# Optimization experiments

Measured on AMD Instinct MI355X. Metric: run time of the kernel, lower is better.

## Reference

```python
import jax, jax.numpy as jnp
import numpy as np
import math


def setup_inputs() -> dict:
    rng = jax.random.key(0)
    k1, k2, k3 = jax.random.split(rng, 3)
    B, L, H, E = 2, 1024, 8, 64
    query = jax.random.normal(k1, (B, L, H, E), dtype=jnp.float32)
    key = jax.random.normal(k2, (B, L, H, E), dtype=jnp.float32)
    value = jax.random.normal(k3, (B, L, H, E), dtype=jnp.float32)
    mask_miss_k = jnp.zeros((B, L), dtype=bool)
    mask_miss_q = jnp.zeros((B, L), dtype=bool)
    pos = jnp.arange(B * L).reshape(B, L)
    causal_mask = 0  # unused by the module body
    # learned scalar parameters (nn.Parameter init values)
    log_gain_gate = jnp.float32(math.log(2.0))
    log_tau_gate = jnp.float32(math.log(0.5))
    log_gain_dir = jnp.float32(math.log(3.0))
    log_tau_dir = jnp.float32(math.log(0.3))
    return {
        "query": query, "key": key, "value": value,
        "mask_miss_k": mask_miss_k, "mask_miss_q": mask_miss_q,
        "pos": pos, "causal_mask": causal_mask,
        "log_gain_gate": log_gain_gate, "log_tau_gate": log_tau_gate,
        "log_gain_dir": log_gain_dir, "log_tau_dir": log_tau_dir,
    }


def reference(query, key, value, mask_miss_k, mask_miss_q, pos, causal_mask,
              log_gain_gate, log_tau_gate, log_gain_dir, log_tau_dir):
    # Multihead path: query (B,L,H,E). Eval mode, dropout p=0, dag_mask=None.
    B, L, H, E = query.shape
    scale = 1.0 / jnp.sqrt(jnp.float32(E))
    # scores: (B,H,L,S) with S == L
    scores = scale * jnp.einsum('blhe,bshe->bhls', query, key)
    scores_t = jnp.swapaxes(scores, -1, -2)
    S_sym = 0.5 * (scores + scores_t)       # symmetric part
    A_anti = 0.5 * (scores - scores_t)      # antisymmetric (Lie) part

    MAX_GAIN = 20.0
    gain_gate = jnp.clip(jnp.exp(log_gain_gate), 1e-3, MAX_GAIN)
    tau_gate = jnp.clip(jnp.exp(log_tau_gate), 1e-3, 10.0)
    gain_dir = jnp.clip(jnp.exp(log_gain_dir), 1e-3, MAX_GAIN)
    tau_dir = jnp.clip(jnp.exp(log_tau_dir), 1e-3, 10.0)

    gamma_att = gain_gate * jnp.tanh(S_sym / tau_gate)
    phi_att = gain_dir * jnp.tanh(A_anti / tau_dir)

    gate_probs = jax.nn.sigmoid(gamma_att)
    dir_probs = jax.nn.sigmoid(phi_att)
    dag_probs = gate_probs * dir_probs

    diag = jnp.eye(L, L, dtype=bool)  # P(i->i) = 0
    dag_probs = jnp.where(diag[None, None], 0.0, dag_probs)
    M = dag_probs  # eval branch; diagonal already zeroed (second fill is a no-op)

    att = jax.nn.relu(jnp.tanh(A_anti * gain_dir / tau_dir)) * M

    # entropy per query position (B,H,L)
    entropy = -jnp.sum(att * jnp.log(jnp.clip(att, 1e-8, None)), axis=-1)
    entropy = jnp.nan_to_num(entropy)

    # dropout p=0 -> identity; nan_to_num is a no-op on finite att
    V = jnp.einsum('bhls,bshd->blhd', att, value)  # (B,L,H,E)
    return V, att, entropy
```

## Files before the change

### kernel.cpp

```cpp
#include <hip/hip_runtime.h>
#include <math.h>

namespace {

typedef __bf16 bf16_t;
typedef bf16_t bf16x8 __attribute__((ext_vector_type(8)));
typedef bf16_t bf16x4 __attribute__((ext_vector_type(4)));
typedef bf16_t bf16x2 __attribute__((ext_vector_type(2)));
typedef float f32x4 __attribute__((ext_vector_type(4)));

constexpr int L = 1024;
constexpr int H = 8;
constexpr int E = 64;
constexpr int HE = H * E;
constexpr int BH = 16;
constexpr size_t PL = (size_t)BH * L * E;
constexpr float LOG2E = 1.4426950408889634f;
constexpr float LN2 = 0.6931471805599453f;

__device__ __forceinline__ float rcp_fast(float x) { return __builtin_amdgcn_rcpf(x); }
__device__ __forceinline__ float exp2_fast(float x) { return __builtin_amdgcn_exp2f(x); }
__device__ __forceinline__ float log2_fast(float x) { return __builtin_amdgcn_logf(x); }
__device__ __forceinline__ f32x4 mfma16(bf16x8 a, bf16x8 b, f32x4 c) {
  return __builtin_amdgcn_mfma_f32_16x16x32_bf16(a, b, c, 0, 0, 0);
}
__device__ __forceinline__ void split4(float4 x, bf16x4& hv, bf16x4& lv) {
  hv[0] = (bf16_t)x.x; lv[0] = (bf16_t)(x.x - (float)hv[0]);
  hv[1] = (bf16_t)x.y; lv[1] = (bf16_t)(x.y - (float)hv[1]);
  hv[2] = (bf16_t)x.z; lv[2] = (bf16_t)(x.z - (float)hv[2]);
  hv[3] = (bf16_t)x.w; lv[3] = (bf16_t)(x.w - (float)hv[3]);
}

__global__ __launch_bounds__(256) void k_prep(
    const float* __restrict__ q, const float* __restrict__ k,
    const float* __restrict__ v, bf16_t* __restrict__ ws,
    float* __restrict__ Vout, float* __restrict__ entr)
{
  const int bid = blockIdx.x;
  if (bid >= 512) {
    const int idx = (bid - 512) * 256 + threadIdx.x;
    const float4 z = make_float4(0.f, 0.f, 0.f, 0.f);
    if (idx < 262144) *(float4*)(Vout + (size_t)idx * 4) = z;
    else              *(float4*)(entr + (size_t)(idx - 262144) * 4) = z;
    return;
  }
  bf16_t* Qh = ws;
  bf16_t* Ql = ws + PL;
  bf16_t* Kh = ws + 2 * PL;
  bf16_t* Kl = ws + 3 * PL;
  bf16_t* VT = ws + 4 * PL;
  const int bh = bid >> 5, chunk = bid & 31;
  const int b = bh >> 3, h = bh & 7;
  const int tid = threadIdx.x, t8 = tid >> 4, c4 = tid & 15;
  __shared__ bf16_t Vb[64][40];

#pragma unroll
  for (int pass = 0; pass < 2; ++pass) {
    const int row = chunk * 32 + pass * 16 + t8;
    const size_t gin = ((size_t)(b * L + row) * H + h) * E + c4 * 4;
    const size_t gout = ((size_t)bh * L + row) * E + c4 * 4;
    float4 q4 = *(const float4*)(q + gin);
    float4 k4 = *(const float4*)(k + gin);
    float4 v4 = *(const float4*)(v + gin);
    bf16x4 hv, lv;
    split4(q4, hv, lv);
    *(bf16x4*)(Qh + gout) = hv; *(bf16x4*)(Ql + gout) = lv;
    split4(k4, hv, lv);
    *(bf16x4*)(Kh + gout) = hv; *(bf16x4*)(Kl + gout) = lv;
    const int sl = pass * 16 + t8;
    Vb[c4 * 4 + 0][sl] = (bf16_t)v4.x;
    Vb[c4 * 4 + 1][sl] = (bf16_t)v4.y;
    Vb[c4 * 4 + 2][sl] = (bf16_t)v4.z;
    Vb[c4 * 4 + 3][sl] = (bf16_t)v4.w;
  }
  __syncthreads();
  {
    const int e = tid >> 2, ch = tid & 3;
    bf16x8 val = *(const bf16x8*)&Vb[e][ch * 8];
    *(bf16x8*)(VT + ((size_t)bh * E + e) * L + chunk * 32 + ch * 8) = val;
  }
}

__global__ __launch_bounds__(256, 3) void k_main(
    const bf16_t* __restrict__ ws,
    float* __restrict__ Vout, float* __restrict__ attg, float* __restrict__ entr,
    const float* __restrict__ p_lgg, const float* __restrict__ p_ltg,
    const float* __restrict__ p_lgd, const float* __restrict__ p_ltd)
{
  const bf16_t* Qh = ws;
  const bf16_t* Ql = ws + PL;
  const bf16_t* Kh = ws + 2 * PL;
  const bf16_t* Kl = ws + 3 * PL;
  const bf16_t* VT = ws + 4 * PL;

  __shared__ __align__(16) char smem[51200];
  bf16_t (*Kh_s)[72] = (bf16_t(*)[72])(smem);
  bf16_t (*Kl_s)[72] = (bf16_t(*)[72])(smem + 9216);
  bf16_t (*Qh_s)[72] = (bf16_t(*)[72])(smem + 18432);
  bf16_t (*Ql_s)[72] = (bf16_t(*)[72])(smem + 27648);
  bf16_t (*Vt_s)[72] = (bf16_t(*)[72])(smem + 36864);
  bf16_t (*attL)[40] = (bf16_t(*)[40])(smem + 46080);

  const int tid = threadIdx.x;
  const int w = tid >> 6, lane = tid & 63;
  const int c = lane & 15, qd = lane >> 4;
  const int lh = w & 1, sh = w >> 1;
  const int wid = blockIdx.x;
  const int xcd = wid & 7, slot = wid >> 3;
  const int bh = xcd * 2 + (slot >> 7);
  const int rsl = slot & 127;
  const int lt = rsl & 31, zb = rsl >> 5;
  const int b = bh >> 3, h = bh & 7;
  const int l0 = lt * 32;

  const float gg = fminf(fmaxf(__expf(p_lgg[0]), 1e-3f), 20.0f);
  const float tg = fminf(fmaxf(__expf(p_ltg[0]), 1e-3f), 10.0f);
  const float gd = fminf(fmaxf(__expf(p_lgd[0]), 1e-3f), 20.0f);
  const float td = fminf(fmaxf(__expf(p_ltd[0]), 1e-3f), 10.0f);
  const float A1 = 0.125f * (1.0f / tg) * LOG2E;
  const float A2 = 0.125f * (1.0f / td) * LOG2E;
  const float A3 = 0.125f * gd * (1.0f / td) * LOG2E;
  const float G1 = -gg * LOG2E, G1m2 = -2.0f * G1;
  const float G2 = -gd * LOG2E, G2m2 = -2.0f * G2;

  bf16x8 qaf[2][2], kaf[2][2];
  {
    const size_t aro = ((size_t)bh * L + l0 + lh * 16 + c) * E;
#pragma unroll
    for (int ks = 0; ks < 2; ++ks) {
      qaf[ks][0] = *(const bf16x8*)(Qh + aro + ks * 32 + qd * 8);
      qaf[ks][1] = *(const bf16x8*)(Ql + aro + ks * 32 + qd * 8);
      kaf[ks][0] = *(const bf16x8*)(Kh + aro + ks * 32 + qd * 8);
      kaf[ks][1] = *(const bf16x8*)(Kl + aro + ks * 32 + qd * 8);
    }
  }

  const int srow = tid >> 2, scol = (tid & 3) * 16;

  bf16x8 kh8a, kh8b, kl8a, kl8b, qh8a, qh8b, ql8a, ql8b, vt8a, vt8b;
  {
    const int s0 = zb * 4 * 64;
    const size_t off = ((size_t)bh * L + s0 + srow) * E + scol;
    kh8a = *(const bf16x8*)(Kh + off);   kh8b = *(const bf16x8*)(Kh + off + 8);
    kl8a = *(const bf16x8*)(Kl + off);   kl8b = *(const bf16x8*)(Kl + off + 8);
    qh8a = *(const bf16x8*)(Qh + off);   qh8b = *(const bf16x8*)(Qh + off + 8);
    ql8a = *(const bf16x8*)(Ql + off);   ql8b = *(const bf16x8*)(Ql + off + 8);
    const size_t voff = ((size_t)bh * E + srow) * L + s0 + scol;
    vt8a = *(const bf16x8*)(VT + voff);  vt8b = *(const bf16x8*)(VT + voff + 8);
  }

  f32x4 accv[4] = {};
  float ent[4] = {0.f, 0.f, 0.f, 0.f};

#pragma unroll
  for (int it = 0; it < 4; ++it) {
    const int s0 = (zb * 4 + it) * 64;
    const int s0n = ((zb * 4 + it + 1) & 15) * 64;

    __syncthreads();
    *(bf16x8*)&Kh_s[srow][scol]     = kh8a;
    *(bf16x8*)&Kh_s[srow][scol + 8] = kh8b;
    *(bf16x8*)&Kl_s[srow][scol]     = kl8a;
    *(bf16x8*)&Kl_s[srow][scol + 8] = kl8b;
    *(bf16x8*)&Qh_s[srow][scol]     = qh8a;
    *(bf16x8*)&Qh_s[srow][scol + 8] = qh8b;
    *(bf16x8*)&Ql_s[srow][scol]     = ql8a;
    *(bf16x8*)&Ql_s[srow][scol + 8] = ql8b;
    *(bf16x8*)&Vt_s[srow][scol]     = vt8a;
    *(bf16x8*)&Vt_s[srow][scol + 8] = vt8b;
    __syncthreads();

    {
      const size_t off = ((size_t)bh * L + s0n + srow) * E + scol;
      kh8a = *(const bf16x8*)(Kh + off);   kh8b = *(const bf16x8*)(Kh + off + 8);
      kl8a = *(const bf16x8*)(Kl + off);   kl8b = *(const bf16x8*)(Kl + off + 8);
      qh8a = *(const bf16x8*)(Qh + off);   qh8b = *(const bf16x8*)(Qh + off + 8);
      ql8a = *(const bf16x8*)(Ql + off);   ql8b = *(const bf16x8*)(Ql + off + 8);
      const size_t voff = ((size_t)bh * E + srow) * L + s0n + scol;
      vt8a = *(const bf16x8*)(VT + voff);  vt8b = *(const bf16x8*)(VT + voff + 8);
    }

    f32x4 acc1[2] = {}, acc2[2] = {};
#pragma unroll
    for (int nt = 0; nt < 2; ++nt) {
      const int brow = sh * 32 + nt * 16 + c;
#pragma unroll
      for (int ks = 0; ks < 2; ++ks) {
        bf16x8 kbh = *(const bf16x8*)&Kh_s[brow][ks * 32 + qd * 8];
        bf16x8 kbl = *(const bf16x8*)&Kl_s[brow][ks * 32 + qd * 8];
        bf16x8 qbh = *(const bf16x8*)&Qh_s[brow][ks * 32 + qd * 8];
        bf16x8 qbl = *(const bf16x8*)&Ql_s[brow][ks * 32 + qd * 8];
        acc1[nt] = mfma16(qaf[ks][0], kbh, acc1[nt]);
        acc1[nt] = mfma16(qaf[ks][0], kbl, acc1[nt]);
        acc1[nt] = mfma16(qaf[ks][1], kbh, acc1[nt]);
        acc2[nt] = mfma16(kaf[ks][0], qbh, acc2[nt]);
        acc2[nt] = mfma16(kaf[ks][1], qbh, acc2[nt]);
        acc2[nt] = mfma16(kaf[ks][0], qbl, acc2[nt]);
      }
    }

    float* arow = attg + ((size_t)bh * L + l0 + lh * 16 + qd * 4) * L + s0 + sh * 32;
#pragma unroll
    for (int nt = 0; nt < 2; ++nt) {
#pragma unroll
      for (int r = 0; r < 4; ++r) {
        float u = acc1[nt][r] + acc2[nt][r];
        float d = acc1[nt][r] - acc2[nt][r];
        float r1 = rcp_fast(exp2_fast(u * A1) + 1.f);
        float gate = rcp_fast(1.f + exp2_fast(fmaf(r1, G1m2, G1)));
        float r2 = rcp_fast(exp2_fast(d * A2) + 1.f);
        float dir  = rcp_fast(1.f + exp2_fast(fmaf(r2, G2m2, G2)));
        float t    = fmaf(rcp_fast(exp2_fast(d * A3) + 1.f), -2.f, 1.f);
        float a = fmaxf(t, 0.0f) * gate * dir;
        ent[r] -= a * log2_fast(fmaxf(a, 1e-8f));
        __builtin_nontemporal_store(a, arow + (size_t)r * L + nt * 16 + c);
        attL[w * 16 + qd * 4 + r][nt * 16 + c] = (bf16_t)a;
      }
    }
    asm volatile("s_waitcnt lgkmcnt(0)" ::: "memory");

    bf16x8 af = *(const bf16x8*)&attL[w * 16 + c][qd * 8];
#pragma unroll
    for (int ne = 0; ne < 4; ++ne) {
      bf16x8 bv = *(const bf16x8*)&Vt_s[ne * 16 + c][sh * 32 + qd * 8];
      accv[ne] = mfma16(af, bv, accv[ne]);
    }
  }

  __syncthreads();
  float (*red)[68] = (float(*)[68])smem;
  if (sh == 1) {
#pragma unroll
    for (int ne = 0; ne < 4; ++ne)
#pragma unroll
      for (int r = 0; r < 4; ++r)
        red[lh * 16 + qd * 4 + r][ne * 16 + c] = accv[ne][r];
  }
  __syncthreads();
  if (sh == 0) {
#pragma unroll
    for (int ne = 0; ne < 4; ++ne)
#pragma unroll
      for (int r = 0; r < 4; ++r) {
        float val = accv[ne][r] + red[lh * 16 + qd * 4 + r][ne * 16 + c];
        atomicAdd(Vout + ((size_t)(b * L + l0 + lh * 16 + qd * 4 + r) * H + h) * E +
                      ne * 16 + c,
                  val);
      }
  }
#pragma unroll
  for (int r = 0; r < 4; ++r) {
    float e = ent[r];
    e += __shfl_xor(e, 1);
    e += __shfl_xor(e, 2);
    e += __shfl_xor(e, 4);
    e += __shfl_xor(e, 8);
    if (c == 0)
      atomicAdd(entr + (size_t)bh * L + l0 + lh * 16 + qd * 4 + r, e * LN2);
  }
}

__device__ __forceinline__ float tanh_fast(float x) {
  return 1.0f - 2.0f * rcp_fast(__expf(2.0f * x) + 1.0f);
}
__device__ __forceinline__ float sigm_fast(float x) {
  return rcp_fast(1.0f + __expf(-x));
}
__device__ __forceinline__ void split_store(bf16_t* hi, bf16_t* lo, float4 x) {
  bf16x4 hv, lv;
  split4(x, hv, lv);
  *(bf16x4*)hi = hv;
  *(bf16x4*)lo = lv;
}

__global__ __launch_bounds__(128, 1) void fused_attn(
    const float* __restrict__ q, const float* __restrict__ kk,
    const float* __restrict__ v,
    float* __restrict__ Vout, float* __restrict__ attg, float* __restrict__ entr,
    const float* __restrict__ p_lgg, const float* __restrict__ p_ltg,
    const float* __restrict__ p_lgd, const float* __restrict__ p_ltd)
{
  constexpr int TM = 32;
  __shared__ bf16_t Qa_hi[TM][72], Qa_lo[TM][72];
  __shared__ bf16_t Ka_hi[TM][72], Ka_lo[TM][72];
  __shared__ bf16_t KQ_hi[64][72], KQ_lo[64][72];
  __shared__ bf16_t Vts[64][72];
  __shared__ float  T2ex[2][64][17];
  __shared__ bf16_t attLs[2][16][72];

  const int tid = threadIdx.x;
  const int w = tid >> 6;
  const int lane = tid & 63;
  const int c = lane & 15;
  const int qd = lane >> 4;
  const int t8 = tid >> 4;
  const int c4 = tid & 15;
  const int lt = blockIdx.x;
  const int bh = blockIdx.y;
  const int b = bh >> 3, h = bh & 7;
  const int l0 = lt * TM;

  const float gg = fminf(fmaxf(__expf(p_lgg[0]), 1e-3f), 20.0f);
  const float tg = fminf(fmaxf(__expf(p_ltg[0]), 1e-3f), 10.0f);
  const float gd = fminf(fmaxf(__expf(p_lgd[0]), 1e-3f), 20.0f);
  const float td = fminf(fmaxf(__expf(p_ltd[0]), 1e-3f), 10.0f);
  const float inv_tg = 1.0f / tg;
  const float inv_td = 1.0f / td;
  const float gd_inv_td = gd * inv_td;

  const float* qlbase = q  + ((size_t)(b * L + l0) * H + h) * E;
  const float* qsbase = q  + ((size_t)b * L * H + h) * E;
  const float* kbase  = kk + ((size_t)b * L * H + h) * E;
  const float* vbase  = v  + ((size_t)b * L * H + h) * E;

#pragma unroll
  for (int i = 0; i < 4; ++i) {
    int r = t8 + 8 * i;
    float4 qa = *(const float4*)(qlbase + (size_t)r * HE + c4 * 4);
    float4 ka = *(const float4*)(kbase + (size_t)(l0 + r) * HE + c4 * 4);
    split_store(&Qa_hi[r][c4 * 4], &Qa_lo[r][c4 * 4], qa);
    split_store(&Ka_hi[r][c4 * 4], &Ka_lo[r][c4 * 4], ka);
  }

  float4 kpre[8], qpre[8];
  float vpre[32];
#pragma unroll
  for (int i = 0; i < 8; ++i)
    kpre[i] = *(const float4*)(kbase + (size_t)(t8 + 8 * i) * HE + c4 * 4);
#pragma unroll
  for (int i = 0; i < 8; ++i)
    qpre[i] = *(const float4*)(qsbase + (size_t)(t8 + 8 * i) * HE + c4 * 4);
#pragma unroll
  for (int j = 0; j < 32; ++j)
    vpre[j] = vbase[(size_t)(w * 32 + j) * HE + lane];

  __syncthreads();

  bf16x8 qaf[2][2], kaf[2][2];
#pragma unroll
  for (int ks = 0; ks < 2; ++ks) {
    qaf[ks][0] = *(const bf16x8*)&Qa_hi[w * 16 + c][ks * 32 + qd * 8];
    qaf[ks][1] = *(const bf16x8*)&Qa_lo[w * 16 + c][ks * 32 + qd * 8];
    kaf[ks][0] = *(const bf16x8*)&Ka_hi[w * 16 + c][ks * 32 + qd * 8];
    kaf[ks][1] = *(const bf16x8*)&Ka_lo[w * 16 + c][ks * 32 + qd * 8];
  }

  f32x4 accv[4] = {};
  float ent[4] = {0.f, 0.f, 0.f, 0.f};
  const int gl_base = l0 + w * 16 + qd * 4;

  for (int it = 0; it < 16; ++it) {
    const int s0 = it * 64;
    const int snext = ((it + 1) & 15) * 64;

    __syncthreads();
#pragma unroll
    for (int i = 0; i < 8; ++i) {
      int r = t8 + 8 * i;
      split_store(&KQ_hi[r][c4 * 4], &KQ_lo[r][c4 * 4], kpre[i]);
    }
#pragma unroll
    for (int j = 0; j < 16; ++j) {
      bf16x2 p;
      p[0] = (bf16_t)vpre[2 * j];
      p[1] = (bf16_t)vpre[2 * j + 1];
      *(bf16x2*)&Vts[lane][w * 32 + 2 * j] = p;
    }
    __syncthreads();

#pragma unroll
    for (int i = 0; i < 8; ++i)
      kpre[i] = *(const float4*)(kbase + (size_t)(snext + t8 + 8 * i) * HE + c4 * 4);
#pragma unroll
    for (int j = 0; j < 32; ++j)
      vpre[j] = vbase[(size_t)(snext + w * 32 + j) * HE + lane];

    f32x4 acc1[4] = {};
#pragma unroll
    for (int nt = 0; nt < 4; ++nt) {
#pragma unroll
      for (int ks = 0; ks < 2; ++ks) {
        bf16x8 bhv = *(const bf16x8*)&KQ_hi[nt * 16 + c][ks * 32 + qd * 8];
        bf16x8 blv = *(const bf16x8*)&KQ_lo[nt * 16 + c][ks * 32 + qd * 8];
        acc1[nt] = mfma16(qaf[ks][0], bhv, acc1[nt]);
        acc1[nt] = mfma16(qaf[ks][0], blv, acc1[nt]);
        acc1[nt] = mfma16(qaf[ks][1], bhv, acc1[nt]);
      }
    }
    __syncthreads();

#pragma unroll
    for (int i = 0; i < 8; ++i) {
      int r = t8 + 8 * i;
      split_store(&KQ_hi[r][c4 * 4], &KQ_lo[r][c4 * 4], qpre[i]);
    }
    __syncthreads();

#pragma unroll
    for (int i = 0; i < 8; ++i)
      qpre[i] = *(const float4*)(qsbase + (size_t)(snext + t8 + 8 * i) * HE + c4 * 4);

    f32x4 acc2[4] = {};
#pragma unroll
    for (int mt = 0; mt < 4; ++mt) {
#pragma unroll
      for (int ks = 0; ks < 2; ++ks) {
        bf16x8 ahv = *(const bf16x8*)&KQ_hi[mt * 16 + c][ks * 32 + qd * 8];
        bf16x8 alv = *(const bf16x8*)&KQ_lo[mt * 16 + c][ks * 32 + qd * 8];
        acc2[mt] = mfma16(ahv, kaf[ks][0], acc2[mt]);
        acc2[mt] = mfma16(ahv, kaf[ks][1], acc2[mt]);
        acc2[mt] = mfma16(alv, kaf[ks][0], acc2[mt]);
      }
    }

#pragma unroll
    for (int mt = 0; mt < 4; ++mt)
#pragma unroll
      for (int r = 0; r < 4; ++r)
        T2ex[w][mt * 16 + qd * 4 + r][c] = acc2[mt][r];
    __syncthreads();

    float* attrow0 = attg + ((size_t)bh * L + gl_base) * L + s0;
#pragma unroll
    for (int nt = 0; nt < 4; ++nt) {
#pragma unroll
      for (int r = 0; r < 4; ++r) {
        float x = 0.125f * acc1[nt][r];
        float y = 0.125f * T2ex[w][nt * 16 + c][qd * 4 + r];
        float Ss = 0.5f * (x + y);
        float Aa = 0.5f * (x - y);
        float gate = sigm_fast(gg * tanh_fast(Ss * inv_tg));
        float dir  = sigm_fast(gd * tanh_fast(Aa * inv_td));
        float t    = tanh_fast(Aa * gd_inv_td);
        float a = fmaxf(t, 0.0f) * gate * dir;
        ent[r] -= a * __logf(fmaxf(a, 1e-8f));
        attrow0[(size_t)r * L + nt * 16 + c] = a;
        attLs[w][qd * 4 + r][nt * 16 + c] = (bf16_t)a;
      }
    }
    __syncthreads();

#pragma unroll
    for (int ks = 0; ks < 2; ++ks) {
      bf16x8 af = *(const bf16x8*)&attLs[w][c][ks * 32 + qd * 8];
#pragma unroll
      for (int ne = 0; ne < 4; ++ne) {
        bf16x8 bfv = *(const bf16x8*)&Vts[ne * 16 + c][ks * 32 + qd * 8];
        accv[ne] = mfma16(af, bfv, accv[ne]);
      }
    }
  }

#pragma unroll
  for (int r = 0; r < 4; ++r) {
    float* vb = Vout + ((size_t)(b * L + gl_base + r) * H + h) * E;
#pragma unroll
    for (int ne = 0; ne < 4; ++ne) vb[ne * 16 + c] = accv[ne][r];
    float e4 = ent[r];
    e4 += __shfl_xor(e4, 1);
    e4 += __shfl_xor(e4, 2);
    e4 += __shfl_xor(e4, 4);
    e4 += __shfl_xor(e4, 8);
    if (c == 0) entr[(size_t)bh * L + gl_base + r] = e4;
  }
}

}

extern "C" void kernel_launch(void* const* d_in, const int* in_sizes, int n_in,
                              void* d_out, int out_size, void* d_ws, size_t ws_size,
                              hipStream_t stream) {
  const float* q = (const float*)d_in[0];
  const float* k = (const float*)d_in[1];
  const float* v = (const float*)d_in[2];
  const float* p_lgg = (const float*)d_in[7];
  const float* p_ltg = (const float*)d_in[8];
  const float* p_lgd = (const float*)d_in[9];
  const float* p_ltd = (const float*)d_in[10];

  float* Vout = (float*)d_out;
  float* att  = Vout + 1048576;
  float* entr = att + 16777216;

  const size_t need = 5 * PL * sizeof(bf16_t);
  if (ws_size >= need) {
    bf16_t* ws = (bf16_t*)d_ws;
    k_prep<<<dim3(1552), 256, 0, stream>>>(q, k, v, ws, Vout, entr);
    k_main<<<dim3(2048), 256, 0, stream>>>(
        ws, Vout, att, entr, p_lgg, p_ltg, p_lgd, p_ltd);
  } else {
    fused_attn<<<dim3(32, 16), 128, 0, stream>>>(
        q, k, v, Vout, att, entr, p_lgg, p_ltg, p_lgd, p_ltd);
  }
}
```

Before: 140.5 us.

## Drop split-S decomposition in main kernel, write outputs directly without atomics

The main kernel previously split the key dimension across 4 blocks per query tile (2048 blocks) and combined partial V and entropy results with atomicAdd, which required a zeroing pass in the prep kernel. Each block now loops over all 16 key tiles itself, so there are 512 blocks, the V and entropy outputs are written with plain stores, and the zero-fill blocks are removed from k_prep. This removes atomic traffic and the memset work, but each block now runs four times longer and there are fewer blocks to spread across the CUs, so latency hiding and load balance may suffer.

```diff
diff --git a/kernel.cpp b/kernel.cpp
--- a/kernel.cpp
+++ b/kernel.cpp
@@ -33,22 +33,14 @@
 
 __global__ __launch_bounds__(256) void k_prep(
     const float* __restrict__ q, const float* __restrict__ k,
-    const float* __restrict__ v, bf16_t* __restrict__ ws,
-    float* __restrict__ Vout, float* __restrict__ entr)
+    const float* __restrict__ v, bf16_t* __restrict__ ws)
 {
-  const int bid = blockIdx.x;
-  if (bid >= 512) {
-    const int idx = (bid - 512) * 256 + threadIdx.x;
-    const float4 z = make_float4(0.f, 0.f, 0.f, 0.f);
-    if (idx < 262144) *(float4*)(Vout + (size_t)idx * 4) = z;
-    else              *(float4*)(entr + (size_t)(idx - 262144) * 4) = z;
-    return;
-  }
   bf16_t* Qh = ws;
   bf16_t* Ql = ws + PL;
   bf16_t* Kh = ws + 2 * PL;
   bf16_t* Kl = ws + 3 * PL;
   bf16_t* VT = ws + 4 * PL;
+  const int bid = blockIdx.x;
   const int bh = bid >> 5, chunk = bid & 31;
   const int b = bh >> 3, h = bh & 7;
   const int tid = threadIdx.x, t8 = tid >> 4, c4 = tid & 15;
@@ -107,9 +99,8 @@
   const int lh = w & 1, sh = w >> 1;
   const int wid = blockIdx.x;
   const int xcd = wid & 7, slot = wid >> 3;
-  const int bh = xcd * 2 + (slot >> 7);
-  const int rsl = slot & 127;
-  const int lt = rsl & 31, zb = rsl >> 5;
+  const int bh = xcd * 2 + (slot >> 5);
+  const int lt = slot & 31;
   const int b = bh >> 3, h = bh & 7;
   const int l0 = lt * 32;
 
@@ -139,23 +130,21 @@
 
   bf16x8 kh8a, kh8b, kl8a, kl8b, qh8a, qh8b, ql8a, ql8b, vt8a, vt8b;
   {
-    const int s0 = zb * 4 * 64;
-    const size_t off = ((size_t)bh * L + s0 + srow) * E + scol;
+    const size_t off = ((size_t)bh * L + srow) * E + scol;
     kh8a = *(const bf16x8*)(Kh + off);   kh8b = *(const bf16x8*)(Kh + off + 8);
     kl8a = *(const bf16x8*)(Kl + off);   kl8b = *(const bf16x8*)(Kl + off + 8);
     qh8a = *(const bf16x8*)(Qh + off);   qh8b = *(const bf16x8*)(Qh + off + 8);
     ql8a = *(const bf16x8*)(Ql + off);   ql8b = *(const bf16x8*)(Ql + off + 8);
-    const size_t voff = ((size_t)bh * E + srow) * L + s0 + scol;
+    const size_t voff = ((size_t)bh * E + srow) * L + scol;
     vt8a = *(const bf16x8*)(VT + voff);  vt8b = *(const bf16x8*)(VT + voff + 8);
   }
 
   f32x4 accv[4] = {};
   float ent[4] = {0.f, 0.f, 0.f, 0.f};
 
-#pragma unroll
-  for (int it = 0; it < 4; ++it) {
-    const int s0 = (zb * 4 + it) * 64;
-    const int s0n = ((zb * 4 + it + 1) & 15) * 64;
+  for (int it = 0; it < 16; ++it) {
+    const int s0 = it * 64;
+    const int s0n = ((it + 1) & 15) * 64;
 
     __syncthreads();
     *(bf16x8*)&Kh_s[srow][scol]     = kh8a;
@@ -229,25 +218,9 @@
 
   __syncthreads();
   float (*red)[68] = (float(*)[68])smem;
-  if (sh == 1) {
-#pragma unroll
-    for (int ne = 0; ne < 4; ++ne)
-#pragma unroll
-      for (int r = 0; r < 4; ++r)
-        red[lh * 16 + qd * 4 + r][ne * 16 + c] = accv[ne][r];
-  }
-  __syncthreads();
-  if (sh == 0) {
-#pragma unroll
-    for (int ne = 0; ne < 4; ++ne)
-#pragma unroll
-      for (int r = 0; r < 4; ++r) {
-        float val = accv[ne][r] + red[lh * 16 + qd * 4 + r][ne * 16 + c];
-        atomicAdd(Vout + ((size_t)(b * L + l0 + lh * 16 + qd * 4 + r) * H + h) * E +
-                      ne * 16 + c,
-                  val);
-      }
-  }
+  float* entE = (float*)(smem + 12288);
+
+  float er[4];
 #pragma unroll
   for (int r = 0; r < 4; ++r) {
     float e = ent[r];
@@ -255,8 +228,34 @@
     e += __shfl_xor(e, 2);
     e += __shfl_xor(e, 4);
     e += __shfl_xor(e, 8);
+    er[r] = e;
+  }
+  if (sh == 1) {
+#pragma unroll
+    for (int ne = 0; ne < 4; ++ne)
+#pragma unroll
+      for (int r = 0; r < 4; ++r)
+        red[lh * 16 + qd * 4 + r][ne * 16 + c] = accv[ne][r];
     if (c == 0)
-      atomicAdd(entr + (size_t)bh * L + l0 + lh * 16 + qd * 4 + r, e * LN2);
+#pragma unroll
+      for (int r = 0; r < 4; ++r)
+        entE[lh * 16 + qd * 4 + r] = er[r];
+  }
+  __syncthreads();
+  if (sh == 0) {
+#pragma unroll
+    for (int ne = 0; ne < 4; ++ne)
+#pragma unroll
+      for (int r = 0; r < 4; ++r) {
+        float val = accv[ne][r] + red[lh * 16 + qd * 4 + r][ne * 16 + c];
+        Vout[((size_t)(b * L + l0 + lh * 16 + qd * 4 + r) * H + h) * E +
+             ne * 16 + c] = val;
+      }
+    if (c == 0)
+#pragma unroll
+      for (int r = 0; r < 4; ++r)
+        entr[(size_t)bh * L + l0 + lh * 16 + qd * 4 + r] =
+            (er[r] + entE[lh * 16 + qd * 4 + r]) * LN2;
   }
 }
 
@@ -485,8 +484,8 @@
   const size_t need = 5 * PL * sizeof(bf16_t);
   if (ws_size >= need) {
     bf16_t* ws = (bf16_t*)d_ws;
-    k_prep<<<dim3(1552), 256, 0, stream>>>(q, k, v, ws, Vout, entr);
-    k_main<<<dim3(2048), 256, 0, stream>>>(
+    k_prep<<<dim3(512), 256, 0, stream>>>(q, k, v, ws);
+    k_main<<<dim3(512), 256, 0, stream>>>(
         ws, Vout, att, entr, p_lgg, p_ltg, p_lgd, p_ltd);
   } else {
     fused_attn<<<dim3(32, 16), 128, 0, stream>>>(
```

Result: no change. 140.0 us (-0.3%).
